# Kernel tuning notes

Measured on AMD Instinct MI355X. Metric: run time of the kernel, lower is better.

The kernel has to match this reference:

```python
import jax, jax.numpy as jnp
import numpy as np

K = 9            # box-filter size per axis
PAD = (K - 1) // 2
KSIZE = K * K * K  # 729


def _box_sum(x):
    """Separable 9x9x9 box sum with zero padding (same math as conv3d with all-ones kernel)."""
    for i in range(3):  # loop over the 3 spatial axes (fixed small structural loop)
        ks = [1, 1, 1]
        ks[i] = K
        pad = [(0, 0)] * 3
        pad[i] = (PAD, PAD)
        kern = jnp.ones((1, 1, *ks), x.dtype)
        x = jax.lax.conv_general_dilated(
            x, kern, window_strides=(1, 1, 1), padding=pad,
            dimension_numbers=('NCDHW', 'OIDHW', 'NCDHW'))
    return x


def setup_inputs() -> dict:
    key = jax.random.key(0)
    k1, k2 = jax.random.split(key)
    shape = (2, 1, 160, 192, 160)
    return {
        'input': jax.random.normal(k1, shape, dtype=jnp.float32),
        'target': jax.random.normal(k2, shape, dtype=jnp.float32),
    }


def reference(input, target):
    # target rescaled from (-1, 1) to (0, 1), as in the torch module
    target = (target + 1.0) * 0.5

    II = input * input
    TT = target * target
    IT = input * target

    T_sum = _box_sum(target)
    I_sum = _box_sum(input)
    TT_sum = _box_sum(TT)
    II_sum = _box_sum(II)
    IT_sum = _box_sum(IT)

    Ihat = I_sum / KSIZE
    That = T_sum / KSIZE

    cross = IT_sum - Ihat * T_sum - That * I_sum + That * Ihat * KSIZE
    T_var = TT_sum - 2.0 * That * T_sum + That * That * KSIZE
    I_var = II_sum - 2.0 * Ihat * I_sum + Ihat * Ihat * KSIZE

    cc = cross * cross / (T_var * I_var + 1e-5)
    return -1.0 * jnp.mean(cc)
```

## Files before the change

### kernel.cpp

```cpp
#include <hip/hip_runtime.h>

namespace {

typedef _Float16 half_t;
typedef _Float16 half2_t __attribute__((ext_vector_type(2)));
typedef _Float16 half4_t __attribute__((ext_vector_type(4)));
typedef _Float16 half8_t __attribute__((ext_vector_type(8)));

constexpr int Wd = 160, Hd = 192, Dd = 160;
constexpr int TX = 16, TY = 16, CZ = 80;
constexpr int HW = Hd * Wd;
constexpr int LIVE = CZ + 8;
constexpr float INV_K = 1.0f / 729.0f;
constexpr float INV_TOT = 1.0f / 9830400.0f;
constexpr int R8 = 17;
constexpr int ROWS = 26;


__global__ __launch_bounds__(256)
void ncc_main(const float* __restrict__ inp, const float* __restrict__ tgt,
              float* __restrict__ out)
{
    __shared__ half8_t xs8[2][ROWS * R8];
    __shared__ half4_t ringAB[9 * 256];
    __shared__ half_t  ringT[9 * 256];
    __shared__ float   red[4];

    const int tid = threadIdx.x;

    const int lin = (int)blockIdx.x + 10 * (int)blockIdx.y + 120 * (int)blockIdx.z;
    const int swz = (lin & 7) * 60 + (lin >> 3);
    const int bx = swz % 10;
    const int by = (swz / 10) % 12;
    const int bz = swz / 120;

    const int n  = bz >> 1;
    const int zc = bz & 1;
    const int x0 = bx * TX, y0 = by * TY, z0 = zc * CZ;

    #pragma unroll
    for (int q = 0; q < 9; ++q) {
        ringAB[q * 256 + tid] = (half4_t)0;
        ringT[q * 256 + tid] = (half_t)0.f;
    }

    const int f = tid % 5;
    const int j = tid / 5;
    const int r = j >> 1, h = j & 1;
    const int gy = y0 - 4 + r;
    const bool yok = (tid < 240) && (gy >= 0) && (gy < Hd);
    const int gyc = min(max(gy, 0), Hd - 1);
    const int gxb = x0 - 4 + 8 * h;
    const bool uI = (f == 0) || (f == 1) || (f == 3);
    const float bI = (f == 0) ? 1.f : 0.f;
    const float bT = (f == 1 || f == 2) ? 0.5f : 0.f;
    const float bC = (f == 1 || f == 2) ? 0.5f : ((f >= 3) ? 1.f : 0.f);

#define DECODE(c) \
    int voff##c; float aI##c, aTC##c; \
    { const int gx = gxb + 4 * c; \
      const float m = (yok && gx >= 0 && gx < Wd) ? 1.f : 0.f; \
      const int gxc = min(max(gx, 0), Wd - 4); \
      voff##c = gyc * Wd + gxc; \
      aI##c = uI ? m : 0.f; aTC##c = uI ? 0.f : 0.5f * m; }
    DECODE(0) DECODE(1) DECODE(2) DECODE(3)
#undef DECODE

    const int nb = n * (Dd * HW);
    const float* baseI = inp + nb;
    const float* baseT = tgt + nb;

    const int stoff = (r * R8 + 8 * h) * 8 + f;
    half_t* const st0 = (half_t*)xs8[0] + stoff;
    half_t* const st1 = (half_t*)xs8[1] + stoff;

    const int xi = tid & 15;
    const int yp = (tid >> 4) & 7;
    const bool p2on = tid < 128;
    const half8_t* const rd8_0 = &xs8[0][(2 * yp) * R8 + xi];
    const half8_t* const rd8_1 = &xs8[1][(2 * yp) * R8 + xi];

    float4 S4a = make_float4(0.f, 0.f, 0.f, 0.f);
    float4 S4b = make_float4(0.f, 0.f, 0.f, 0.f);
    float STa = 0.f, STb = 0.f, acc = 0.f;

#define DECL_SET(S) \
    float4 S##I0, S##I1, S##I2, S##I3, S##T0, S##T1, S##T2, S##T3; \
    S##I0 = S##I1 = S##I2 = S##I3 = make_float4(0.f, 0.f, 0.f, 0.f); \
    S##T0 = S##T1 = S##T2 = S##T3 = S##I0;
    DECL_SET(A) DECL_SET(B)
#undef DECL_SET

#define PRELOAD(S, zz) { \
    const float* pI = baseI + (zz) * HW; \
    const float* pT = baseT + (zz) * HW; \
    S##I0 = *(const float4*)(pI + voff0); S##T0 = *(const float4*)(pT + voff0); \
    S##I1 = *(const float4*)(pI + voff1); S##T1 = *(const float4*)(pT + voff1); \
    S##I2 = *(const float4*)(pI + voff2); S##T2 = *(const float4*)(pT + voff2); \
    S##I3 = *(const float4*)(pI + voff3); S##T3 = *(const float4*)(pT + voff3); }

    if (z0 - 4 >= 0) PRELOAD(A, z0 - 4)
    if (z0 - 3 >= 0) PRELOAD(B, z0 - 3)

#define PRODC(S, c, P0, P1, P2, P3) { \
    P0 = fmaf(S##I##c.x, aI##c, fmaf(S##T##c.x, aTC##c, aTC##c)) * fmaf(S##I##c.x, bI, fmaf(S##T##c.x, bT, bC)); \
    P1 = fmaf(S##I##c.y, aI##c, fmaf(S##T##c.y, aTC##c, aTC##c)) * fmaf(S##I##c.y, bI, fmaf(S##T##c.y, bT, bC)); \
    P2 = fmaf(S##I##c.z, aI##c, fmaf(S##T##c.z, aTC##c, aTC##c)) * fmaf(S##I##c.z, bI, fmaf(S##T##c.z, bT, bC)); \
    P3 = fmaf(S##I##c.w, aI##c, fmaf(S##T##c.w, aTC##c, aTC##c)) * fmaf(S##I##c.w, bI, fmaf(S##T##c.w, bT, bC)); }

#define SLICE_BODY(SET) { \
    const int zi = z0 - 4 + s; \
    const bool zok = (zi >= 0) && (zi < Dd);         \
    const int sl = u % 9;                            \
    const int pb = u & 1;                            \
    float o0, o1, o2, o3, o4, o5, o6, o7; \
    if (zok) { \
        float p0, p1, p2, p3, p4, p5, p6, p7; \
        float p8, p9, p10, p11, p12, p13, p14, p15; \
        PRODC(SET, 0, p0,  p1,  p2,  p3) \
        PRODC(SET, 1, p4,  p5,  p6,  p7) \
        PRODC(SET, 2, p8,  p9,  p10, p11) \
        PRODC(SET, 3, p12, p13, p14, p15) \
        float ss = p0 + p1 + p2 + p3 + p4 + p5 + p6 + p7 + p8; \
        o0 = ss; \
        ss += p9  - p0; o1 = ss; \
        ss += p10 - p1; o2 = ss; \
        ss += p11 - p2; o3 = ss; \
        ss += p12 - p3; o4 = ss; \
        ss += p13 - p4; o5 = ss; \
        ss += p14 - p5; o6 = ss; \
        ss += p15 - p6; o7 = ss; \
    } \
    {    \
        const int zi2 = z0 - 2 + s; \
        if ((s + 2) < LIVE && zi2 >= 0 && zi2 < Dd) PRELOAD(SET, zi2) \
    } \
    if (zok) { \
        half_t* const st = pb ? st1 : st0; \
        st[0]  = (half_t)o0; st[8]  = (half_t)o1; \
        st[16] = (half_t)o2; st[24] = (half_t)o3; \
        st[32] = (half_t)o4; st[40] = (half_t)o5; \
        st[48] = (half_t)o6; st[56] = (half_t)o7; \
    } \
    __syncthreads();                                 \
    half2_t a01_0 = (half2_t)0, a23_0 = (half2_t)0; \
    half2_t a01_1 = (half2_t)0, a23_1 = (half2_t)0; \
    half_t aT0 = (half_t)0.f, aT1 = (half_t)0.f; \
    if (zok && p2on) { \
        const half8_t* const rd8 = pb ? rd8_1 : rd8_0; \
        const half8_t w0 = rd8[0]; \
        const half8_t w9 = rd8[9 * R8]; \
        half2_t m01 = (half2_t)0, m23 = (half2_t)0, m4 = (half2_t)0; \
        _Pragma("unroll") \
        for (int k = 1; k < 9; ++k) { \
            const half8_t w = rd8[k * R8]; \
            const half2_t* wp = (const half2_t*)&w; \
            m01 += wp[0]; m23 += wp[1]; m4 += wp[2]; \
        } \
        const half2_t* w0p = (const half2_t*)&w0; \
        const half2_t* w9p = (const half2_t*)&w9; \
        a01_0 = m01 + w0p[0]; a23_0 = m23 + w0p[1]; aT0 = m4.x + w0p[2].x; \
        a01_1 = m01 + w9p[0]; a23_1 = m23 + w9p[1]; aT1 = m4.x + w9p[2].x; \
    } \
    if (p2on) {  \
        half8_t* const rAB8 = (half8_t*)&ringAB[sl * 256 + 2 * tid]; \
        half2_t* const rT  = (half2_t*)&ringT[sl * 256 + 2 * tid]; \
        const half8_t oA = *rAB8; \
        const half2_t oT = *rT; \
        S4a.x += (float)a01_0.x - (float)oA[0]; \
        S4a.y += (float)a01_0.y - (float)oA[1]; \
        S4a.z += (float)a23_0.x - (float)oA[2]; \
        S4a.w += (float)a23_0.y - (float)oA[3]; \
        STa   += (float)aT0 - (float)oT.x; \
        S4b.x += (float)a01_1.x - (float)oA[4]; \
        S4b.y += (float)a01_1.y - (float)oA[5]; \
        S4b.z += (float)a23_1.x - (float)oA[6]; \
        S4b.w += (float)a23_1.y - (float)oA[7]; \
        STb   += (float)aT1 - (float)oT.y; \
        const half8_t nA = {a01_0.x, a01_0.y, a23_0.x, a23_0.y, \
                            a01_1.x, a01_1.y, a23_1.x, a23_1.y}; \
        *rAB8 = nA; \
        const half2_t nT = {aT0, aT1}; \
        *rT = nT; \
    } \
    if (s >= 8 && p2on) {                            \
        { const float sii = S4a.x, sit = S4a.y, stt = S4a.z, si = S4a.w, stv = STa; \
          const float cross = sit - si * stv * INV_K; \
          const float tvar  = stt - stv * stv * INV_K; \
          const float ivar  = sii - si  * si  * INV_K; \
          acc += cross * cross * __builtin_amdgcn_rcpf(tvar * ivar + 1e-5f); } \
        { const float sii = S4b.x, sit = S4b.y, stt = S4b.z, si = S4b.w, stv = STb; \
          const float cross = sit - si * stv * INV_K; \
          const float tvar  = stt - stv * stv * INV_K; \
          const float ivar  = sii - si  * si  * INV_K; \
          acc += cross * cross * __builtin_amdgcn_rcpf(tvar * ivar + 1e-5f); } \
    } }

    for (int tb = 0; tb < 90; tb += 18) {
        #pragma unroll
        for (int u = 0; u < 18; ++u) {
            const int s = tb + u;
            if (s < LIVE) {
                if ((u & 1) == 0) SLICE_BODY(A)
                else              SLICE_BODY(B)
            }
        }
    }
#undef SLICE_BODY
#undef PRELOAD
#undef PRODC

    #pragma unroll
    for (int off = 32; off > 0; off >>= 1) acc += __shfl_down(acc, off, 64);
    if ((tid & 63) == 0) red[tid >> 6] = acc;
    __syncthreads();
    if (tid == 0) {
        const float tot = red[0] + red[1] + red[2] + red[3];
        atomicAdd(out, -tot * INV_TOT);
    }
}

}

extern "C" void kernel_launch(void* const* d_in, const int* in_sizes, int n_in,
                              void* d_out, int out_size, void* d_ws, size_t ws_size,
                              hipStream_t stream)
{
    const float* inp = (const float*)d_in[0];
    const float* tgt = (const float*)d_in[1];
    float* out = (float*)d_out;

    hipMemsetAsync(d_out, 0, sizeof(float), stream);
    dim3 grid(Wd / TX, Hd / TY, 2 * (Dd / CZ));
    ncc_main<<<grid, 256, 0, stream>>>(inp, tgt, out);
}
```

Measured before the change: 160.4 us.

## Specialize producer warps and software-pipeline x-window production against consumer

Result: faster. 152.2 us (-5.1%).

```diff
diff --git a/kernel.cpp b/kernel.cpp
--- a/kernel.cpp
+++ b/kernel.cpp
@@ -14,7 +14,7 @@
 constexpr float INV_K = 1.0f / 729.0f;
 constexpr float INV_TOT = 1.0f / 9830400.0f;
 constexpr int R8 = 17;
-constexpr int ROWS = 26;
+constexpr int ROWS = 24;
 
 
 __global__ __launch_bounds__(256)
@@ -44,35 +44,32 @@
         ringT[q * 256 + tid] = (half_t)0.f;
     }
 
-    const int f = tid % 5;
-    const int j = tid / 5;
-    const int r = j >> 1, h = j & 1;
+    const bool isProd = (tid >= 128) && (tid < 224);
+    const int up = (tid >= 128) ? (tid - 128) : 0;
+    const int r  = (up < 96) ? (up >> 2) : 0;
+    const int hq = up & 3;
+    const int h  = hq >> 1, qx = hq & 1;
     const int gy = y0 - 4 + r;
-    const bool yok = (tid < 240) && (gy >= 0) && (gy < Hd);
+    const bool yok = (gy >= 0) && (gy < Hd);
     const int gyc = min(max(gy, 0), Hd - 1);
-    const int gxb = x0 - 4 + 8 * h;
-    const bool uI = (f == 0) || (f == 1) || (f == 3);
-    const float bI = (f == 0) ? 1.f : 0.f;
-    const float bT = (f == 1 || f == 2) ? 0.5f : 0.f;
-    const float bC = (f == 1 || f == 2) ? 0.5f : ((f >= 3) ? 1.f : 0.f);
+    const int gxs = x0 - 4 + 8 * h + 4 * qx;
 
 #define DECODE(c) \
-    int voff##c; float aI##c, aTC##c; \
-    { const int gx = gxb + 4 * c; \
-      const float m = (yok && gx >= 0 && gx < Wd) ? 1.f : 0.f; \
+    int voff##c; float m##c; \
+    { const int gx = gxs + 4 * (c); \
+      m##c = (yok && gx >= 0 && gx < Wd) ? 1.f : 0.f; \
       const int gxc = min(max(gx, 0), Wd - 4); \
-      voff##c = gyc * Wd + gxc; \
-      aI##c = uI ? m : 0.f; aTC##c = uI ? 0.f : 0.5f * m; }
-    DECODE(0) DECODE(1) DECODE(2) DECODE(3)
+      voff##c = gyc * Wd + gxc; }
+    DECODE(0) DECODE(1) DECODE(2)
 #undef DECODE
 
     const int nb = n * (Dd * HW);
     const float* baseI = inp + nb;
     const float* baseT = tgt + nb;
 
-    const int stoff = (r * R8 + 8 * h) * 8 + f;
-    half_t* const st0 = (half_t*)xs8[0] + stoff;
-    half_t* const st1 = (half_t*)xs8[1] + stoff;
+    const int col0 = 8 * h + 4 * qx;
+    half_t* const sb0 = (half_t*)xs8[0] + (r * R8 + col0) * 8;
+    half_t* const sb1 = (half_t*)xs8[1] + (r * R8 + col0) * 8;
 
     const int xi = tid & 15;
     const int yp = (tid >> 4) & 7;
@@ -84,131 +81,140 @@
     float4 S4b = make_float4(0.f, 0.f, 0.f, 0.f);
     float STa = 0.f, STb = 0.f, acc = 0.f;
 
-#define DECL_SET(S) \
-    float4 S##I0, S##I1, S##I2, S##I3, S##T0, S##T1, S##T2, S##T3; \
-    S##I0 = S##I1 = S##I2 = S##I3 = make_float4(0.f, 0.f, 0.f, 0.f); \
-    S##T0 = S##T1 = S##T2 = S##T3 = S##I0;
-    DECL_SET(A) DECL_SET(B)
-#undef DECL_SET
-
-#define PRELOAD(S, zz) { \
+    float4 SI0, SI1, SI2, ST0, ST1, ST2;
+    SI0 = SI1 = SI2 = ST0 = ST1 = ST2 = make_float4(0.f, 0.f, 0.f, 0.f);
+
+#define PRELOAD(zz) { \
     const float* pI = baseI + (zz) * HW; \
     const float* pT = baseT + (zz) * HW; \
-    S##I0 = *(const float4*)(pI + voff0); S##T0 = *(const float4*)(pT + voff0); \
-    S##I1 = *(const float4*)(pI + voff1); S##T1 = *(const float4*)(pT + voff1); \
-    S##I2 = *(const float4*)(pI + voff2); S##T2 = *(const float4*)(pT + voff2); \
-    S##I3 = *(const float4*)(pI + voff3); S##T3 = *(const float4*)(pT + voff3); }
-
-    if (z0 - 4 >= 0) PRELOAD(A, z0 - 4)
-    if (z0 - 3 >= 0) PRELOAD(B, z0 - 3)
-
-#define PRODC(S, c, P0, P1, P2, P3) { \
-    P0 = fmaf(S##I##c.x, aI##c, fmaf(S##T##c.x, aTC##c, aTC##c)) * fmaf(S##I##c.x, bI, fmaf(S##T##c.x, bT, bC)); \
-    P1 = fmaf(S##I##c.y, aI##c, fmaf(S##T##c.y, aTC##c, aTC##c)) * fmaf(S##I##c.y, bI, fmaf(S##T##c.y, bT, bC)); \
-    P2 = fmaf(S##I##c.z, aI##c, fmaf(S##T##c.z, aTC##c, aTC##c)) * fmaf(S##I##c.z, bI, fmaf(S##T##c.z, bT, bC)); \
-    P3 = fmaf(S##I##c.w, aI##c, fmaf(S##T##c.w, aTC##c, aTC##c)) * fmaf(S##I##c.w, bI, fmaf(S##T##c.w, bT, bC)); }
-
-#define SLICE_BODY(SET) { \
-    const int zi = z0 - 4 + s; \
-    const bool zok = (zi >= 0) && (zi < Dd);         \
-    const int sl = u % 9;                            \
-    const int pb = u & 1;                            \
-    float o0, o1, o2, o3, o4, o5, o6, o7; \
-    if (zok) { \
-        float p0, p1, p2, p3, p4, p5, p6, p7; \
-        float p8, p9, p10, p11, p12, p13, p14, p15; \
-        PRODC(SET, 0, p0,  p1,  p2,  p3) \
-        PRODC(SET, 1, p4,  p5,  p6,  p7) \
-        PRODC(SET, 2, p8,  p9,  p10, p11) \
-        PRODC(SET, 3, p12, p13, p14, p15) \
-        float ss = p0 + p1 + p2 + p3 + p4 + p5 + p6 + p7 + p8; \
-        o0 = ss; \
-        ss += p9  - p0; o1 = ss; \
-        ss += p10 - p1; o2 = ss; \
-        ss += p11 - p2; o3 = ss; \
-        ss += p12 - p3; o4 = ss; \
-        ss += p13 - p4; o5 = ss; \
-        ss += p14 - p5; o6 = ss; \
-        ss += p15 - p6; o7 = ss; \
+    SI0 = *(const float4*)(pI + voff0); ST0 = *(const float4*)(pT + voff0); \
+    SI1 = *(const float4*)(pI + voff1); ST1 = *(const float4*)(pT + voff1); \
+    SI2 = *(const float4*)(pI + voff2); ST2 = *(const float4*)(pT + voff2); }
+
+#define F4E(v, e) ((e) == 0 ? (v).x : ((e) == 1 ? (v).y : ((e) == 2 ? (v).z : (v).w)))
+
+#define WIN4(PP, W) { \
+    float ss = PP[0] + PP[1] + PP[2] + PP[3] + PP[4] + PP[5] + PP[6] + PP[7] + PP[8]; \
+    W[0] = ss; ss += PP[9]  - PP[0]; W[1] = ss; \
+               ss += PP[10] - PP[1]; W[2] = ss; \
+               ss += PP[11] - PP[2]; W[3] = ss; }
+
+#define PRODUCE(SBP) { \
+    float Im[12], Tr[12], p[12]; \
+    float wII[4], wIT[4], wTT[4], wI[4], wT[4]; \
+    _Pragma("unroll") \
+    for (int e = 0; e < 4; ++e) { \
+        Im[e]     = F4E(SI0, e) * m0;  Tr[e]     = fmaf(F4E(ST0, e), 0.5f, 0.5f); \
+        Im[4 + e] = F4E(SI1, e) * m1;  Tr[4 + e] = fmaf(F4E(ST1, e), 0.5f, 0.5f); \
+        Im[8 + e] = F4E(SI2, e) * m2;  Tr[8 + e] = fmaf(F4E(ST2, e), 0.5f, 0.5f); } \
+    _Pragma("unroll") \
+    for (int i = 0; i < 12; ++i) \
+        p[i] = Im[i] * F4E((i < 4 ? SI0 : (i < 8 ? SI1 : SI2)), i & 3); \
+    WIN4(p, wII) \
+    _Pragma("unroll") \
+    for (int i = 0; i < 12; ++i) p[i] = Im[i] * Tr[i]; \
+    WIN4(p, wIT) \
+    WIN4(Im, wI) \
+    _Pragma("unroll") \
+    for (int i = 0; i < 12; ++i) Im[i] = Tr[i] * (i < 4 ? m0 : (i < 8 ? m1 : m2)); \
+    _Pragma("unroll") \
+    for (int i = 0; i < 12; ++i) p[i] = Im[i] * Tr[i]; \
+    WIN4(p, wTT) \
+    WIN4(Im, wT) \
+    _Pragma("unroll") \
+    for (int cc = 0; cc < 4; ++cc) { \
+        const half2_t v01 = {(half_t)wII[cc], (half_t)wIT[cc]}; \
+        const half2_t v23 = {(half_t)wTT[cc], (half_t)wI[cc]}; \
+        ((half2_t*)(SBP))[cc * 4]     = v01; \
+        ((half2_t*)(SBP))[cc * 4 + 1] = v23; \
+        (SBP)[cc * 8 + 4] = (half_t)wT[cc]; } }
+
+    if (isProd) {
+        if (z0 - 4 >= 0) { PRELOAD(z0 - 4) PRODUCE(sb0) }
+        if (z0 - 3 >= 0) PRELOAD(z0 - 3)
+    }
+    __syncthreads();
+
+#define STEP_BODY(UU) { \
+    const int k = tb + (UU); \
+    if (isProd) { \
+        const int zi1 = z0 - 3 + k;              \
+        if ((k + 1) < LIVE && zi1 >= 0 && zi1 < Dd) { \
+            if (((UU) & 1) == 0) PRODUCE(sb1) else PRODUCE(sb0) \
+        } \
+        const int zi2 = z0 - 2 + k;              \
+        if ((k + 2) < LIVE && zi2 >= 0 && zi2 < Dd) PRELOAD(zi2) \
     } \
-    {    \
-        const int zi2 = z0 - 2 + s; \
-        if ((s + 2) < LIVE && zi2 >= 0 && zi2 < Dd) PRELOAD(SET, zi2) \
+    {  \
+        const int zi = z0 - 4 + k; \
+        const bool zok = (zi >= 0) && (zi < Dd); \
+        half2_t a01_0 = (half2_t)0, a23_0 = (half2_t)0; \
+        half2_t a01_1 = (half2_t)0, a23_1 = (half2_t)0; \
+        half_t aT0 = (half_t)0.f, aT1 = (half_t)0.f; \
+        if (zok && p2on) { \
+            const half8_t* const rd8 = (((UU) & 1) != 0) ? rd8_1 : rd8_0; \
+            const half8_t w0 = rd8[0]; \
+            const half8_t w9 = rd8[9 * R8]; \
+            half2_t m01 = (half2_t)0, m23 = (half2_t)0, m4 = (half2_t)0; \
+            _Pragma("unroll") \
+            for (int kk = 1; kk < 9; ++kk) { \
+                const half8_t w = rd8[kk * R8]; \
+                const half2_t* wp = (const half2_t*)&w; \
+                m01 += wp[0]; m23 += wp[1]; m4 += wp[2]; \
+            } \
+            const half2_t* w0p = (const half2_t*)&w0; \
+            const half2_t* w9p = (const half2_t*)&w9; \
+            a01_0 = m01 + w0p[0]; a23_0 = m23 + w0p[1]; aT0 = m4.x + w0p[2].x; \
+            a01_1 = m01 + w9p[0]; a23_1 = m23 + w9p[1]; aT1 = m4.x + w9p[2].x; \
+        } \
+        if (p2on) { \
+            const int sl = (UU) % 9;             \
+            half8_t* const rAB8 = (half8_t*)&ringAB[sl * 256 + 2 * tid]; \
+            half2_t* const rT  = (half2_t*)&ringT[sl * 256 + 2 * tid]; \
+            const half8_t oA = *rAB8; \
+            const half2_t oT = *rT; \
+            S4a.x += (float)a01_0.x - (float)oA[0]; \
+            S4a.y += (float)a01_0.y - (float)oA[1]; \
+            S4a.z += (float)a23_0.x - (float)oA[2]; \
+            S4a.w += (float)a23_0.y - (float)oA[3]; \
+            STa   += (float)aT0 - (float)oT.x; \
+            S4b.x += (float)a01_1.x - (float)oA[4]; \
+            S4b.y += (float)a01_1.y - (float)oA[5]; \
+            S4b.z += (float)a23_1.x - (float)oA[6]; \
+            S4b.w += (float)a23_1.y - (float)oA[7]; \
+            STb   += (float)aT1 - (float)oT.y; \
+            const half8_t nA = {a01_0.x, a01_0.y, a23_0.x, a23_0.y, \
+                                a01_1.x, a01_1.y, a23_1.x, a23_1.y}; \
+            *rAB8 = nA; \
+            const half2_t nT = {aT0, aT1}; \
+            *rT = nT; \
+        } \
+        if (k >= 8 && p2on) {                    \
+            { const float sii = S4a.x, sit = S4a.y, stt = S4a.z, si = S4a.w, stv = STa; \
+              const float cross = sit - si * stv * INV_K; \
+              const float tvar  = stt - stv * stv * INV_K; \
+              const float ivar  = sii - si  * si  * INV_K; \
+              acc += cross * cross * __builtin_amdgcn_rcpf(tvar * ivar + 1e-5f); } \
+            { const float sii = S4b.x, sit = S4b.y, stt = S4b.z, si = S4b.w, stv = STb; \
+              const float cross = sit - si * stv * INV_K; \
+              const float tvar  = stt - stv * stv * INV_K; \
+              const float ivar  = sii - si  * si  * INV_K; \
+              acc += cross * cross * __builtin_amdgcn_rcpf(tvar * ivar + 1e-5f); } \
+        } \
     } \
-    if (zok) { \
-        half_t* const st = pb ? st1 : st0; \
-        st[0]  = (half_t)o0; st[8]  = (half_t)o1; \
-        st[16] = (half_t)o2; st[24] = (half_t)o3; \
-        st[32] = (half_t)o4; st[40] = (half_t)o5; \
-        st[48] = (half_t)o6; st[56] = (half_t)o7; \
-    } \
-    __syncthreads();                                 \
-    half2_t a01_0 = (half2_t)0, a23_0 = (half2_t)0; \
-    half2_t a01_1 = (half2_t)0, a23_1 = (half2_t)0; \
-    half_t aT0 = (half_t)0.f, aT1 = (half_t)0.f; \
-    if (zok && p2on) { \
-        const half8_t* const rd8 = pb ? rd8_1 : rd8_0; \
-        const half8_t w0 = rd8[0]; \
-        const half8_t w9 = rd8[9 * R8]; \
-        half2_t m01 = (half2_t)0, m23 = (half2_t)0, m4 = (half2_t)0; \
-        _Pragma("unroll") \
-        for (int k = 1; k < 9; ++k) { \
-            const half8_t w = rd8[k * R8]; \
-            const half2_t* wp = (const half2_t*)&w; \
-            m01 += wp[0]; m23 += wp[1]; m4 += wp[2]; \
-        } \
-        const half2_t* w0p = (const half2_t*)&w0; \
-        const half2_t* w9p = (const half2_t*)&w9; \
-        a01_0 = m01 + w0p[0]; a23_0 = m23 + w0p[1]; aT0 = m4.x + w0p[2].x; \
-        a01_1 = m01 + w9p[0]; a23_1 = m23 + w9p[1]; aT1 = m4.x + w9p[2].x; \
-    } \
-    if (p2on) {  \
-        half8_t* const rAB8 = (half8_t*)&ringAB[sl * 256 + 2 * tid]; \
-        half2_t* const rT  = (half2_t*)&ringT[sl * 256 + 2 * tid]; \
-        const half8_t oA = *rAB8; \
-        const half2_t oT = *rT; \
-        S4a.x += (float)a01_0.x - (float)oA[0]; \
-        S4a.y += (float)a01_0.y - (float)oA[1]; \
-        S4a.z += (float)a23_0.x - (float)oA[2]; \
-        S4a.w += (float)a23_0.y - (float)oA[3]; \
-        STa   += (float)aT0 - (float)oT.x; \
-        S4b.x += (float)a01_1.x - (float)oA[4]; \
-        S4b.y += (float)a01_1.y - (float)oA[5]; \
-        S4b.z += (float)a23_1.x - (float)oA[6]; \
-        S4b.w += (float)a23_1.y - (float)oA[7]; \
-        STb   += (float)aT1 - (float)oT.y; \
-        const half8_t nA = {a01_0.x, a01_0.y, a23_0.x, a23_0.y, \
-                            a01_1.x, a01_1.y, a23_1.x, a23_1.y}; \
-        *rAB8 = nA; \
-        const half2_t nT = {aT0, aT1}; \
-        *rT = nT; \
-    } \
-    if (s >= 8 && p2on) {                            \
-        { const float sii = S4a.x, sit = S4a.y, stt = S4a.z, si = S4a.w, stv = STa; \
-          const float cross = sit - si * stv * INV_K; \
-          const float tvar  = stt - stv * stv * INV_K; \
-          const float ivar  = sii - si  * si  * INV_K; \
-          acc += cross * cross * __builtin_amdgcn_rcpf(tvar * ivar + 1e-5f); } \
-        { const float sii = S4b.x, sit = S4b.y, stt = S4b.z, si = S4b.w, stv = STb; \
-          const float cross = sit - si * stv * INV_K; \
-          const float tvar  = stt - stv * stv * INV_K; \
-          const float ivar  = sii - si  * si  * INV_K; \
-          acc += cross * cross * __builtin_amdgcn_rcpf(tvar * ivar + 1e-5f); } \
-    } }
+    __syncthreads(); }
 
     for (int tb = 0; tb < 90; tb += 18) {
         #pragma unroll
-        for (int u = 0; u < 18; ++u) {
-            const int s = tb + u;
-            if (s < LIVE) {
-                if ((u & 1) == 0) SLICE_BODY(A)
-                else              SLICE_BODY(B)
-            }
+        for (int uu = 0; uu < 18; ++uu) {
+            if (tb + uu < LIVE) STEP_BODY(uu)
         }
     }
-#undef SLICE_BODY
+#undef STEP_BODY
+#undef PRODUCE
+#undef WIN4
+#undef F4E
 #undef PRELOAD
-#undef PRODC
 
     #pragma unroll
     for (int off = 32; off > 0; off >>= 1) acc += __shfl_down(acc, off, 64);
```
